# Kernel tuning notes

Measured on AMD Instinct MI355X. Metric: run time of the kernel, lower is better.

## Reference

```python
import jax, jax.numpy as jnp
import numpy as np

N_NODES = 100000
N_EDGES = 1280000
IN_DIM = 64
HID = 64
OUT_DIM = 2
N_GRAPHS = 1000
BN_EPS = 1e-5


def setup_inputs() -> dict:
    key = jax.random.key(0)
    ks = jax.random.split(key, 16)
    x = jax.random.normal(ks[0], (N_NODES, IN_DIM), dtype=jnp.float32)
    edge_index = jax.random.randint(ks[1], (2, N_EDGES), 0, N_NODES, dtype=jnp.int64)
    batch = jnp.sort(jax.random.randint(ks[2], (N_NODES,), 0, N_GRAPHS, dtype=jnp.int64))
    # He-init linear weights (stored as [in, out] so forward is x @ W)
    def he(k, fan_in, fan_out):
        return jax.random.normal(k, (fan_in, fan_out), dtype=jnp.float32) * np.sqrt(2.0 / fan_in)
    return {
        "x": x,
        "edge_index": edge_index,
        "batch": batch,
        "bn_in_g": jnp.ones((IN_DIM,), jnp.float32),
        "bn_in_b": jnp.zeros((IN_DIM,), jnp.float32),
        "W1": he(ks[3], IN_DIM, HID), "b1": jnp.zeros((HID,), jnp.float32),
        "g1": jnp.ones((HID,), jnp.float32), "be1": jnp.zeros((HID,), jnp.float32),
        "W2": he(ks[4], HID, HID), "b2": jnp.zeros((HID,), jnp.float32),
        "g2": jnp.ones((HID,), jnp.float32), "be2": jnp.zeros((HID,), jnp.float32),
        "Wout": he(ks[5], HID, OUT_DIM), "bout": jnp.zeros((OUT_DIM,), jnp.float32),
    }


def _batchnorm(x, g, b):
    # training-mode BN over the node dimension (biased variance, as torch uses for normalization)
    m = jnp.mean(x, axis=0)
    v = jnp.mean(jnp.square(x - m), axis=0)
    return (x - m) * jax.lax.rsqrt(v + BN_EPS) * g + b


def _gcn_norm(edge_index, n):
    # PyG GCNConv normalization with added self-loops:
    # norm_e = deg[src]^-1/2 * deg[dst]^-1/2, deg computed on A + I over targets.
    row = jnp.concatenate([edge_index[0], jnp.arange(n, dtype=edge_index.dtype)])
    col = jnp.concatenate([edge_index[1], jnp.arange(n, dtype=edge_index.dtype)])
    deg = jax.ops.segment_sum(jnp.ones_like(col, dtype=jnp.float32), col, num_segments=n)
    dinv = jnp.where(deg > 0, jax.lax.rsqrt(deg), 0.0)
    norm = dinv[row] * dinv[col]
    return row, col, norm


def _gcn_conv(x, W, b, row, col, norm, n):
    h = x @ W                                   # [N, out]
    msg = h[row] * norm[:, None]                # gather over edges (incl. self-loops)
    agg = jax.ops.segment_sum(msg, col, num_segments=n)
    return agg + b


def reference(x, edge_index, batch, bn_in_g, bn_in_b, W1, b1, g1, be1, W2, b2, g2, be2, Wout, bout):
    n = x.shape[0]
    row, col, norm = _gcn_norm(edge_index, n)
    h = _batchnorm(x, bn_in_g, bn_in_b)         # input BN (dropout = identity in eval)
    h = _gcn_conv(h, W1, b1, row, col, norm, n)
    h = _batchnorm(jax.nn.relu(h), g1, be1)
    h = _gcn_conv(h, W2, b2, row, col, norm, n)
    h = _batchnorm(jax.nn.relu(h), g2, be2)
    # global mean pool per graph
    sums = jax.ops.segment_sum(h, batch, num_segments=N_GRAPHS)
    cnts = jax.ops.segment_sum(jnp.ones((n,), h.dtype), batch, num_segments=N_GRAPHS)
    pooled = sums / jnp.maximum(cnts, 1.0)[:, None]
    return pooled @ Wout + bout                 # [N_GRAPHS, OUT_DIM]
```

## Files before the change

kernel.cpp:

```cpp
#include <hip/hip_runtime.h>
#include <math.h>

#define N_NODES 100000
#define N_EDGES 1280000
#define DIM 64
#define N_GRAPHS 1000
#define BN_EPS 1e-5f
#define NB 392
#define P1B 256
#define P1E 5000
#define SB 400
#define WIN 128
#define NWIN (N_EDGES / WIN)
#define GU 8
#define NSLOT 32

__device__ __forceinline__ unsigned int bf16_rtn2(float a, float b) {
    unsigned int ua = __float_as_uint(a);
    unsigned int ub = __float_as_uint(b);
    ua = (ua + 0x7FFFu + ((ua >> 16) & 1u)) >> 16;
    ub = (ub + 0x7FFFu + ((ub >> 16) & 1u)) >> 16;
    return ua | (ub << 16);
}
__device__ __forceinline__ unsigned short bf16r(float a) {
    unsigned int u = __float_as_uint(a);
    return (unsigned short)((u + 0x7FFFu + ((u >> 16) & 1u)) >> 16);
}
__device__ __forceinline__ float bfup(unsigned short u) {
    return __uint_as_float(((unsigned int)u) << 16);
}

__global__ __launch_bounds__(256) void k_p1hist(const int* __restrict__ ei,
                                                const int* __restrict__ batch,
                                                const float* __restrict__ X,
                                                int* __restrict__ bh,
                                                int* __restrict__ start,
                                                float* __restrict__ gsum,
                                                float* __restrict__ gsumsq) {
    int t = threadIdx.x;
    if (blockIdx.x < P1B) {
        __shared__ int hist[NB];
        for (int b = t; b < NB; b += 256) hist[b] = 0;
        __syncthreads();
        int e0 = blockIdx.x * P1E;
        #pragma unroll 4
        for (int e = e0 + t; e < e0 + P1E; e += 256)
            atomicAdd(&hist[ei[N_EDGES + e] >> 8], 1);
        __syncthreads();
        for (int b = t; b < NB; b += 256) bh[b * P1B + blockIdx.x] = hist[b];
    } else if (blockIdx.x < P1B + SB) {
        int grp = blockIdx.x - P1B;
        int j = t & 63, rg = t >> 6;
        int base = grp * 250;
        float s = 0.f, s2 = 0.f;
        for (int i = base + rg; i < base + 250; i += 4) {
            float v = X[i * DIM + j];
            s += v; s2 += v * v;
        }
        __shared__ float ls[256], ls2[256];
        ls[t] = s; ls2[t] = s2;
        __syncthreads();
        if (t < 64) {
            int slot = (grp & (NSLOT - 1)) * DIM;
            s  = ls[j]  + ls[64 + j]  + ls[128 + j]  + ls[192 + j];
            s2 = ls2[j] + ls2[64 + j] + ls2[128 + j] + ls2[192 + j];
            atomicAdd(&gsum[slot + j], s);
            atomicAdd(&gsumsq[slot + j], s2);
        }
    } else {
        int i = (blockIdx.x - P1B - SB) * 256 + t;
        if (i < N_NODES) {
            int cur = batch[i];
            if (i == 0) { for (int q = 0; q <= cur; q++) start[q] = 0; }
            else {
                int prev = batch[i - 1];
                for (int q = prev + 1; q <= cur; q++) start[q] = i;
            }
            if (i == N_NODES - 1)
                for (int q = cur + 1; q <= N_GRAPHS; q++) start[q] = N_NODES;
        }
    }
}

__global__ void k_scan1(const int* __restrict__ bh, int* __restrict__ iscan,
                        int* __restrict__ bsum) {
    __shared__ int ls[256];
    int i = blockIdx.x * 256 + threadIdx.x;
    int v = bh[i];
    ls[threadIdx.x] = v;
    __syncthreads();
    for (int off = 1; off < 256; off <<= 1) {
        int tv = (threadIdx.x >= off) ? ls[threadIdx.x - off] : 0;
        __syncthreads();
        ls[threadIdx.x] += tv;
        __syncthreads();
    }
    iscan[i] = ls[threadIdx.x];
    if (threadIdx.x == 255) bsum[blockIdx.x] = ls[255];
}

__global__ void k_scan2(const int* __restrict__ bsum, int* __restrict__ boff) {
    __shared__ int ls[512];
    int t = threadIdx.x;
    int v0 = (t < NB) ? bsum[t] : 0;
    ls[t] = v0;
    __syncthreads();
    for (int off = 1; off < 512; off <<= 1) {
        int v = (t >= off) ? ls[t - off] : 0;
        __syncthreads();
        ls[t] += v;
        __syncthreads();
    }
    if (t < NB) boff[t] = ls[t] - v0;
}

__global__ __launch_bounds__(256) void k_p1scat(const int* __restrict__ ei,
                                                const int* __restrict__ bh,
                                                const int* __restrict__ iscan,
                                                const int* __restrict__ boff,
                                                int* __restrict__ tmp) {
    __shared__ int cur[NB];
    int blk = blockIdx.x;
    for (int b = threadIdx.x; b < NB; b += 256) {
        int i = b * P1B + blk;
        cur[b] = boff[b] + iscan[i] - bh[i];
    }
    __syncthreads();
    int e0 = blk * P1E;
    for (int e = e0 + threadIdx.x; e < e0 + P1E; e += 256) {
        int r = ei[e], c = ei[N_EDGES + e];
        int pos = atomicAdd(&cur[c >> 8], 1);
        tmp[pos] = (r << 8) | (c & 255);
    }
}

__global__ __launch_bounds__(256) void k_p2a(const int* __restrict__ tmp,
                                             const int* __restrict__ bh,
                                             const int* __restrict__ iscan,
                                             const int* __restrict__ boff,
                                             int* __restrict__ rowstart,
                                             float* __restrict__ dinv,
                                             int* __restrict__ winnode,
                                             float* __restrict__ C) {
    int b = blockIdx.x, t = threadIdx.x;
    int bstart = boff[b] + iscan[b * 256] - bh[b * 256];
    int bend = (b == NB - 1) ? N_EDGES
                             : (boff[b + 1] + iscan[(b + 1) * 256] - bh[(b + 1) * 256]);
    __shared__ int cnt[256], scn[256];
    cnt[t] = 0;
    __syncthreads();
    for (int e = bstart + t; e < bend; e += 256)
        atomicAdd(&cnt[tmp[e] & 255], 1);
    __syncthreads();
    scn[t] = cnt[t];
    __syncthreads();
    for (int off = 1; off < 256; off <<= 1) {
        int v = (t >= off) ? scn[t - off] : 0;
        __syncthreads();
        scn[t] += v;
        __syncthreads();
    }
    int node = b * 256 + t;
    int deg = cnt[t];
    int rs = bstart + scn[t] - deg;
    bool span = false;
    if (node <= N_NODES) rowstart[node] = rs;
    if (node < N_NODES) {
        dinv[node] = 1.0f / sqrtf((float)(deg + 1));
        int re = rs + deg;
        for (int w = (rs + WIN - 1) / WIN; w * WIN < re; ++w) winnode[w] = node;
        span = (deg > 0) && (rs / WIN != (re - 1) / WIN);
    }
    int lane = t & 63;
    int wbase = b * 256 + (t & ~63);
    unsigned long long m = __ballot(span);
    while (m) {
        int bit = __builtin_ctzll(m);
        m &= m - 1;
        C[(size_t)(wbase + bit) * DIM + lane] = 0.f;
    }
}

__global__ __launch_bounds__(256) void k_p2b(const int* __restrict__ tmp,
                                             const int* __restrict__ bh,
                                             const int* __restrict__ iscan,
                                             const int* __restrict__ boff,
                                             const int* __restrict__ rowstart,
                                             int* __restrict__ csr) {
    int b = blockIdx.x, t = threadIdx.x;
    int bstart = boff[b] + iscan[b * 256] - bh[b * 256];
    int bend = (b == NB - 1) ? N_EDGES
                             : (boff[b + 1] + iscan[(b + 1) * 256] - bh[(b + 1) * 256]);
    __shared__ int curs[256];
    int node = b * 256 + t;
    curs[t] = (node < N_NODES) ? rowstart[node] : 0;
    __syncthreads();
    for (int e = bstart + t; e < bend; e += 256) {
        int rec = tmp[e];
        int pos = atomicAdd(&curs[rec & 255], 1);
        csr[pos] = (int)((unsigned)rec >> 8);
    }
}

__global__ void k_bnfold(float* __restrict__ gsum, float* __restrict__ gsumsq,
                         const float* __restrict__ g, const float* __restrict__ b,
                         const float* __restrict__ W,
                         float* __restrict__ scale, float* __restrict__ cshift) {
    int j = threadIdx.x;
    float ms = 0.f, m2 = 0.f;
    for (int k = 0; k < NSLOT; k++) {
        ms += gsum[k * DIM + j];   gsum[k * DIM + j] = 0.f;
        m2 += gsumsq[k * DIM + j]; gsumsq[k * DIM + j] = 0.f;
    }
    float mean = ms * (1.0f / N_NODES);
    float var  = m2 * (1.0f / N_NODES) - mean * mean;
    float inv  = 1.0f / sqrtf(var + BN_EPS);
    float sc   = g[j] * inv;
    scale[j] = sc;
    __shared__ float shl[64];
    shl[j] = b[j] - mean * sc;
    __syncthreads();
    float s = 0.f;
    for (int k = 0; k < DIM; k++) s += shl[k] * W[k * DIM + j];
    cshift[j] = s;
}

__global__ void k_bnfinal(const float* __restrict__ gsum, const float* __restrict__ gsumsq,
                          const float* __restrict__ g, const float* __restrict__ b,
                          float* __restrict__ scale, float* __restrict__ shift) {
    int j = threadIdx.x;
    float ms = 0.f, m2 = 0.f;
    for (int k = 0; k < NSLOT; k++) { ms += gsum[k * DIM + j]; m2 += gsumsq[k * DIM + j]; }
    float mean = ms * (1.0f / N_NODES);
    float var  = m2 * (1.0f / N_NODES) - mean * mean;
    float inv  = 1.0f / sqrtf(var + BN_EPS);
    float sc   = g[j] * inv;
    scale[j] = sc;
    shift[j] = b[j] - mean * sc;
}

__global__ __launch_bounds__(256) void k_gemm_f32(const float* __restrict__ X,
                                                  const float* __restrict__ W,
                                                  const float* __restrict__ scale,
                                                  const float* __restrict__ cshift,
                                                  const float* __restrict__ dinv,
                                                  unsigned short* __restrict__ T) {
    __shared__ float Wl[64 * 64];
    __shared__ float Al[64 * 65];
    for (int t = threadIdx.x; t < 4096; t += 256) Wl[t] = W[t] * scale[t >> 6];
    int row0 = blockIdx.x * 64;
    for (int t = threadIdx.x; t < 4096; t += 256) {
        int r = t >> 6, k = t & 63;
        int i = row0 + r;
        Al[r * 65 + k] = (i < N_NODES) ? X[(size_t)i * DIM + k] : 0.f;
    }
    __syncthreads();
    int r = threadIdx.x & 63;
    int q = threadIdx.x >> 6;
    float acc[16];
    #pragma unroll
    for (int jj = 0; jj < 16; jj++) acc[jj] = cshift[q * 16 + jj];
    #pragma unroll 4
    for (int k = 0; k < 64; k++) {
        float a = Al[r * 65 + k];
        const float4* wv = (const float4*)&Wl[k * 64 + q * 16];
        float4 w0 = wv[0], w1 = wv[1], w2 = wv[2], w3 = wv[3];
        acc[0]  += a * w0.x; acc[1]  += a * w0.y; acc[2]  += a * w0.z; acc[3]  += a * w0.w;
        acc[4]  += a * w1.x; acc[5]  += a * w1.y; acc[6]  += a * w1.z; acc[7]  += a * w1.w;
        acc[8]  += a * w2.x; acc[9]  += a * w2.y; acc[10] += a * w2.z; acc[11] += a * w2.w;
        acc[12] += a * w3.x; acc[13] += a * w3.y; acc[14] += a * w3.z; acc[15] += a * w3.w;
    }
    int i = row0 + r;
    if (i < N_NODES) {
        float dv = dinv[i];
        unsigned int pk[8];
        #pragma unroll
        for (int jj = 0; jj < 8; jj++)
            pk[jj] = bf16_rtn2(acc[2 * jj] * dv, acc[2 * jj + 1] * dv);
        uint4* outv = (uint4*)&T[(size_t)i * DIM + q * 16];
        outv[0] = make_uint4(pk[0], pk[1], pk[2], pk[3]);
        outv[1] = make_uint4(pk[4], pk[5], pk[6], pk[7]);
    }
}

__global__ __launch_bounds__(256) void k_gemm_b16(const unsigned short* __restrict__ X,
                                                  const float* __restrict__ W,
                                                  const float* __restrict__ scale,
                                                  const float* __restrict__ cshift,
                                                  const float* __restrict__ dinv,
                                                  unsigned short* __restrict__ T) {
    __shared__ float Wl[64 * 64];
    __shared__ float Al[64 * 65];
    for (int t = threadIdx.x; t < 4096; t += 256) Wl[t] = W[t] * scale[t >> 6];
    int row0 = blockIdx.x * 64;
    for (int t = threadIdx.x; t < 4096; t += 256) {
        int r = t >> 6, k = t & 63;
        int i = row0 + r;
        Al[r * 65 + k] = (i < N_NODES) ? bfup(X[(size_t)i * DIM + k]) : 0.f;
    }
    __syncthreads();
    int r = threadIdx.x & 63;
    int q = threadIdx.x >> 6;
    float acc[16];
    #pragma unroll
    for (int jj = 0; jj < 16; jj++) acc[jj] = cshift[q * 16 + jj];
    #pragma unroll 4
    for (int k = 0; k < 64; k++) {
        float a = Al[r * 65 + k];
        const float4* wv = (const float4*)&Wl[k * 64 + q * 16];
        float4 w0 = wv[0], w1 = wv[1], w2 = wv[2], w3 = wv[3];
        acc[0]  += a * w0.x; acc[1]  += a * w0.y; acc[2]  += a * w0.z; acc[3]  += a * w0.w;
        acc[4]  += a * w1.x; acc[5]  += a * w1.y; acc[6]  += a * w1.z; acc[7]  += a * w1.w;
        acc[8]  += a * w2.x; acc[9]  += a * w2.y; acc[10] += a * w2.z; acc[11] += a * w2.w;
        acc[12] += a * w3.x; acc[13] += a * w3.y; acc[14] += a * w3.z; acc[15] += a * w3.w;
    }
    int i = row0 + r;
    if (i < N_NODES) {
        float dv = dinv[i];
        unsigned int pk[8];
        #pragma unroll
        for (int jj = 0; jj < 8; jj++)
            pk[jj] = bf16_rtn2(acc[2 * jj] * dv, acc[2 * jj + 1] * dv);
        uint4* outv = (uint4*)&T[(size_t)i * DIM + q * 16];
        outv[0] = make_uint4(pk[0], pk[1], pk[2], pk[3]);
        outv[1] = make_uint4(pk[4], pk[5], pk[6], pk[7]);
    }
}

__global__ __launch_bounds__(256) void k_gather1(const unsigned short* __restrict__ T,
                                                 const float* __restrict__ dinv,
                                                 const int* __restrict__ rowstart,
                                                 const int* __restrict__ winnode,
                                                 const int* __restrict__ csr,
                                                 const float* __restrict__ bias,
                                                 float* __restrict__ C,
                                                 unsigned short* __restrict__ H,
                                                 float* __restrict__ gsum,
                                                 float* __restrict__ gsumsq) {
    int lane = threadIdx.x & 63;
    int w = blockIdx.x * 4 + (threadIdx.x >> 6);
    float bb = bias[lane];
    float s = 0.f, s2 = 0.f;
    int e = w * WIN;
    const int eend = e + WIN;
    int i  = __builtin_amdgcn_readfirstlane(winnode[w]);
    int re = __builtin_amdgcn_readfirstlane(rowstart[i + 1]);
    bool part = __builtin_amdgcn_readfirstlane(rowstart[i]) < e;
    float acc = 0.f;
    for (; e < eend; e += GU) {
        int src[GU];
        int eu = __builtin_amdgcn_readfirstlane(e);
        #pragma unroll
        for (int u = 0; u < GU; u++) src[u] = csr[eu + u];
        float tv[GU];
        #pragma unroll
        for (int u = 0; u < GU; u++) tv[u] = bfup(T[(size_t)src[u] * DIM + lane]);
        #pragma unroll
        for (int u = 0; u < GU; u++) {
            while (e + u == re) {
                if (part) { atomicAdd(&C[(size_t)i * DIM + lane], acc); part = false; }
                else {
                    float di = dinv[i];
                    float h = fmaxf((acc + bfup(T[(size_t)i * DIM + lane])) * di + bb, 0.f);
                    H[(size_t)i * DIM + lane] = bf16r(h);
                    s += h; s2 += h * h;
                }
                acc = 0.f; ++i;
                re = __builtin_amdgcn_readfirstlane(rowstart[i + 1]);
            }
            acc += tv[u];
        }
    }
    if (part || re > eend) atomicAdd(&C[(size_t)i * DIM + lane], acc);
    else {
        float di = dinv[i];
        float h = fmaxf((acc + bfup(T[(size_t)i * DIM + lane])) * di + bb, 0.f);
        H[(size_t)i * DIM + lane] = bf16r(h);
        s += h; s2 += h * h;
    }
    __shared__ float ls[256], ls2[256];
    ls[threadIdx.x] = s; ls2[threadIdx.x] = s2;
    __syncthreads();
    if (threadIdx.x < 64) {
        int j = threadIdx.x;
        int slot = (blockIdx.x & (NSLOT - 1)) * DIM;
        atomicAdd(&gsum[slot + j],   ls[j] + ls[64 + j] + ls[128 + j] + ls[192 + j]);
        atomicAdd(&gsumsq[slot + j], ls2[j] + ls2[64 + j] + ls2[128 + j] + ls2[192 + j]);
    }
}

__global__ __launch_bounds__(256) void k_gather2(const unsigned short* __restrict__ T,
                                                 const float* __restrict__ dinv,
                                                 const int* __restrict__ rowstart,
                                                 const int* __restrict__ winnode,
                                                 const int* __restrict__ csr,
                                                 const float* __restrict__ bias,
                                                 const int* __restrict__ batch,
                                                 float* __restrict__ C,
                                                 float* __restrict__ pool,
                                                 float* __restrict__ gsum,
                                                 float* __restrict__ gsumsq) {
    int lane = threadIdx.x & 63;
    int w = blockIdx.x * 4 + (threadIdx.x >> 6);
    float bb = bias[lane];
    float s = 0.f, s2 = 0.f, ps = 0.f;
    int cur_g = -1;
    int e = w * WIN;
    const int eend = e + WIN;
    int i  = __builtin_amdgcn_readfirstlane(winnode[w]);
    int re = __builtin_amdgcn_readfirstlane(rowstart[i + 1]);
    bool part = __builtin_amdgcn_readfirstlane(rowstart[i]) < e;
    float acc = 0.f;
    for (; e < eend; e += GU) {
        int src[GU];
        int eu = __builtin_amdgcn_readfirstlane(e);
        #pragma unroll
        for (int u = 0; u < GU; u++) src[u] = csr[eu + u];
        float tv[GU];
        #pragma unroll
        for (int u = 0; u < GU; u++) tv[u] = bfup(T[(size_t)src[u] * DIM + lane]);
        #pragma unroll
        for (int u = 0; u < GU; u++) {
            while (e + u == re) {
                if (part) { atomicAdd(&C[(size_t)i * DIM + lane], acc); part = false; }
                else {
                    float di = dinv[i];
                    float h = fmaxf((acc + bfup(T[(size_t)i * DIM + lane])) * di + bb, 0.f);
                    s += h; s2 += h * h;
                    int g = batch[i];
                    if (g != cur_g) {
                        if (cur_g >= 0) atomicAdd(&pool[(size_t)cur_g * DIM + lane], ps);
                        ps = 0.f; cur_g = g;
                    }
                    ps += h;
                }
                acc = 0.f; ++i;
                re = __builtin_amdgcn_readfirstlane(rowstart[i + 1]);
            }
            acc += tv[u];
        }
    }
    if (part || re > eend) atomicAdd(&C[(size_t)i * DIM + lane], acc);
    else {
        float di = dinv[i];
        float h = fmaxf((acc + bfup(T[(size_t)i * DIM + lane])) * di + bb, 0.f);
        s += h; s2 += h * h;
        int g = batch[i];
        if (g != cur_g) {
            if (cur_g >= 0) atomicAdd(&pool[(size_t)cur_g * DIM + lane], ps);
            ps = 0.f; cur_g = g;
        }
        ps += h;
    }
    if (cur_g >= 0) atomicAdd(&pool[(size_t)cur_g * DIM + lane], ps);
    __shared__ float ls[256], ls2[256];
    ls[threadIdx.x] = s; ls2[threadIdx.x] = s2;
    __syncthreads();
    if (threadIdx.x < 64) {
        int j = threadIdx.x;
        int slot = (blockIdx.x & (NSLOT - 1)) * DIM;
        atomicAdd(&gsum[slot + j],   ls[j] + ls[64 + j] + ls[128 + j] + ls[192 + j]);
        atomicAdd(&gsumsq[slot + j], ls2[j] + ls2[64 + j] + ls2[128 + j] + ls2[192 + j]);
    }
}

__global__ __launch_bounds__(256) void k_strad1(float* __restrict__ C,
                                                const unsigned short* __restrict__ T,
                                                const float* __restrict__ dinv,
                                                const int* __restrict__ rowstart,
                                                const int* __restrict__ winnode,
                                                const float* __restrict__ bias,
                                                unsigned short* __restrict__ H,
                                                float* __restrict__ gsum,
                                                float* __restrict__ gsumsq) {
    int lane = threadIdx.x & 63;
    int wv = threadIdx.x >> 6;
    float bb = bias[lane];
    float s = 0.f, s2 = 0.f;
    __shared__ int anyw;
    if (threadIdx.x == 0) anyw = 0;
    __syncthreads();
    if (blockIdx.x < NWIN / 4) {
        int w = blockIdx.x * 4 + wv;
        int n = winnode[w];
        int rs = rowstart[n];
        if (w == rs / WIN + 1) {
            float di = dinv[n];
            float c = C[(size_t)n * DIM + lane];
            C[(size_t)n * DIM + lane] = 0.f;
            float h = fmaxf((c + bfup(T[(size_t)n * DIM + lane])) * di + bb, 0.f);
            H[(size_t)n * DIM + lane] = bf16r(h);
            s += h; s2 += h * h;
            anyw = 1;
        }
    } else {
        int base = (blockIdx.x - NWIN / 4) * 256 + wv * 64;
        int nb = base + lane;
        int d0 = 0;
        if (nb < N_NODES)
            d0 = (rowstart[nb + 1] == rowstart[nb]) && ((rowstart[nb] & (WIN - 1)) == 0);
        unsigned long long m = __ballot(d0);
        while (m) {
            int b = __builtin_ctzll(m);
            m &= m - 1;
            int n = base + b;
            float di = dinv[n];
            float h = fmaxf(bfup(T[(size_t)n * DIM + lane]) * di + bb, 0.f);
            H[(size_t)n * DIM + lane] = bf16r(h);
            s += h; s2 += h * h;
            anyw = 1;
        }
    }
    __shared__ float ls[256], ls2[256];
    ls[threadIdx.x] = s; ls2[threadIdx.x] = s2;
    __syncthreads();
    if (anyw && threadIdx.x < 64) {
        int j = threadIdx.x;
        int slot = (blockIdx.x & (NSLOT - 1)) * DIM;
        atomicAdd(&gsum[slot + j],   ls[j] + ls[64 + j] + ls[128 + j] + ls[192 + j]);
        atomicAdd(&gsumsq[slot + j], ls2[j] + ls2[64 + j] + ls2[128 + j] + ls2[192 + j]);
    }
}

__global__ __launch_bounds__(256) void k_strad2(const float* __restrict__ C,
                                                const unsigned short* __restrict__ T,
                                                const float* __restrict__ dinv,
                                                const int* __restrict__ rowstart,
                                                const int* __restrict__ winnode,
                                                const float* __restrict__ bias,
                                                const int* __restrict__ batch,
                                                float* __restrict__ pool,
                                                float* __restrict__ gsum,
                                                float* __restrict__ gsumsq) {
    int lane = threadIdx.x & 63;
    int wv = threadIdx.x >> 6;
    float bb = bias[lane];
    float s = 0.f, s2 = 0.f;
    __shared__ int anyw;
    if (threadIdx.x == 0) anyw = 0;
    __syncthreads();
    if (blockIdx.x < NWIN / 4) {
        int w = blockIdx.x * 4 + wv;
        int n = winnode[w];
        int rs = rowstart[n];
        if (w == rs / WIN + 1) {
            float di = dinv[n];
            float h = fmaxf((C[(size_t)n * DIM + lane]
                             + bfup(T[(size_t)n * DIM + lane])) * di + bb, 0.f);
            s += h; s2 += h * h;
            atomicAdd(&pool[(size_t)batch[n] * DIM + lane], h);
            anyw = 1;
        }
    } else {
        int base = (blockIdx.x - NWIN / 4) * 256 + wv * 64;
        int nb = base + lane;
        int d0 = 0;
        if (nb < N_NODES)
            d0 = (rowstart[nb + 1] == rowstart[nb]) && ((rowstart[nb] & (WIN - 1)) == 0);
        unsigned long long m = __ballot(d0);
        while (m) {
            int b = __builtin_ctzll(m);
            m &= m - 1;
            int n = base + b;
            float di = dinv[n];
            float h = fmaxf(bfup(T[(size_t)n * DIM + lane]) * di + bb, 0.f);
            s += h; s2 += h * h;
            atomicAdd(&pool[(size_t)batch[n] * DIM + lane], h);
            anyw = 1;
        }
    }
    __shared__ float ls[256], ls2[256];
    ls[threadIdx.x] = s; ls2[threadIdx.x] = s2;
    __syncthreads();
    if (anyw && threadIdx.x < 64) {
        int j = threadIdx.x;
        int slot = (blockIdx.x & (NSLOT - 1)) * DIM;
        atomicAdd(&gsum[slot + j],   ls[j] + ls[64 + j] + ls[128 + j] + ls[192 + j]);
        atomicAdd(&gsumsq[slot + j], ls2[j] + ls2[64 + j] + ls2[128 + j] + ls2[192 + j]);
    }
}

__global__ void k_final(const float* __restrict__ pool, const int* __restrict__ start,
                        const float* __restrict__ scale, const float* __restrict__ shift,
                        const float* __restrict__ Wout, const float* __restrict__ bout,
                        float* __restrict__ out) {
    int g = blockIdx.x;
    int l = threadIdx.x;
    float c = fmaxf((float)(start[g + 1] - start[g]), 1.f);
    float p = (pool[g * DIM + l] / c) * scale[l] + shift[l];
    float a0 = p * Wout[l * 2 + 0];
    float a1 = p * Wout[l * 2 + 1];
    #pragma unroll
    for (int off = 32; off; off >>= 1) {
        a0 += __shfl_down(a0, off, 64);
        a1 += __shfl_down(a1, off, 64);
    }
    if (l == 0) {
        out[g * 2 + 0] = a0 + bout[0];
        out[g * 2 + 1] = a1 + bout[1];
    }
}

extern "C" void kernel_launch(void* const* d_in, const int* in_sizes, int n_in,
                              void* d_out, int out_size, void* d_ws, size_t ws_size,
                              hipStream_t stream) {
    (void)in_sizes; (void)n_in; (void)out_size; (void)ws_size;
    const float* x       = (const float*)d_in[0];
    const int*   ei      = (const int*)d_in[1];
    const int*   batch   = (const int*)d_in[2];
    const float* bn_in_g = (const float*)d_in[3];
    const float* bn_in_b = (const float*)d_in[4];
    const float* W1      = (const float*)d_in[5];
    const float* b1      = (const float*)d_in[6];
    const float* g1      = (const float*)d_in[7];
    const float* be1     = (const float*)d_in[8];
    const float* W2      = (const float*)d_in[9];
    const float* b2      = (const float*)d_in[10];
    const float* g2      = (const float*)d_in[11];
    const float* be2     = (const float*)d_in[12];
    const float* Wout    = (const float*)d_in[13];
    const float* bout    = (const float*)d_in[14];
    float* out = (float*)d_out;

    char* p = (char*)d_ws;
    float* C = (float*)p;                   p += (size_t)N_NODES * DIM * 4;
    unsigned short* H = (unsigned short*)p; p += (size_t)N_NODES * DIM * 2;
    unsigned short* T = (unsigned short*)p; p += (size_t)N_NODES * DIM * 2;
    int* csr = (int*)p;                     p += (size_t)N_EDGES * 4;
    float* dinv = (float*)p;                p += N_NODES * 4;
    int* bh = (int*)p;                      p += NB * P1B * 4;
    int* iscan = (int*)p;                   p += NB * P1B * 4;
    int* rowstart = (int*)p;                p += (N_NODES + 2) * 4;
    int* winnode = (int*)p;                 p += NWIN * 4;
    int* bsum = (int*)p;                    p += NB * 4;
    int* boff = (int*)p;                    p += NB * 4;
    int* start = (int*)p;                   p += (N_GRAPHS + 2) * 4;
    float* gsum = (float*)p;                p += NSLOT * DIM * 4;
    float* gsumsq = (float*)p;              p += NSLOT * DIM * 4;
    float* scale = (float*)p;               p += DIM * 4;
    float* shift = (float*)p;               p += DIM * 4;
    float* cshift = (float*)p;              p += DIM * 4;
    float* pool = (float*)p;                p += (size_t)N_GRAPHS * DIM * 4;
    int* tmp = (int*)H;

    hipMemsetAsync(gsum, 0, 2 * NSLOT * DIM * sizeof(float), stream);
    hipMemsetAsync(pool, 0, (size_t)N_GRAPHS * DIM * sizeof(float), stream);
    k_p1hist<<<P1B + SB + 392, 256, 0, stream>>>(ei, batch, x, bh, start, gsum, gsumsq);
    k_scan1<<<NB, 256, 0, stream>>>(bh, iscan, bsum);
    k_scan2<<<1, 512, 0, stream>>>(bsum, boff);
    k_p1scat<<<P1B, 256, 0, stream>>>(ei, bh, iscan, boff, tmp);
    k_p2a<<<NB, 256, 0, stream>>>(tmp, bh, iscan, boff, rowstart, dinv, winnode, C);
    k_p2b<<<NB, 256, 0, stream>>>(tmp, bh, iscan, boff, rowstart, csr);

    k_bnfold<<<1, 64, 0, stream>>>(gsum, gsumsq, bn_in_g, bn_in_b, W1, scale, cshift);
    k_gemm_f32<<<(N_NODES + 63) / 64, 256, 0, stream>>>(x, W1, scale, cshift, dinv, T);
    k_gather1<<<NWIN / 4, 256, 0, stream>>>(T, dinv, rowstart, winnode, csr, b1,
                                            C, H, gsum, gsumsq);
    k_strad1<<<NWIN / 4 + 392, 256, 0, stream>>>(C, T, dinv, rowstart, winnode, b1,
                                                 H, gsum, gsumsq);

    k_bnfold<<<1, 64, 0, stream>>>(gsum, gsumsq, g1, be1, W2, scale, cshift);
    k_gemm_b16<<<(N_NODES + 63) / 64, 256, 0, stream>>>(H, W2, scale, cshift, dinv, T);
    k_gather2<<<NWIN / 4, 256, 0, stream>>>(T, dinv, rowstart, winnode, csr, b2,
                                            batch, C, pool, gsum, gsumsq);
    k_strad2<<<NWIN / 4 + 392, 256, 0, stream>>>(C, T, dinv, rowstart, winnode, b2,
                                                 batch, pool, gsum, gsumsq);

    k_bnfinal<<<1, 64, 0, stream>>>(gsum, gsumsq, g2, be2, scale, shift);
    k_final<<<N_GRAPHS, 64, 0, stream>>>(pool, start, scale, shift, Wout, bout, out);
}
```

Baseline: 329.8 us.

## Gather four edges per wave with 8-byte lane loads and preloaded row metadata

The gather kernels now split each wave into four 16-lane groups. Each group handles a different edge and loads 4 bf16 features as one uint2, so one wave covers four edges per load and the partial sums are combined with cross-lane shuffles. CSR indices are loaded once per window and spread with ds_swizzle. rowstart, dinv and batch for the next 64 nodes are preloaded and read with readlane instead of scalar loads. The window shrinks to 64 edges, doubling the number of waves, which adds more straddle atomics and more complex per-edge branching in exchange for fewer, wider memory requests.

```diff
diff --git a/kernel.cpp b/kernel.cpp
--- a/kernel.cpp
+++ b/kernel.cpp
@@ -10,9 +10,8 @@
 #define P1B 256
 #define P1E 5000
 #define SB 400
-#define WIN 128
+#define WIN 64
 #define NWIN (N_EDGES / WIN)
-#define GU 8
 #define NSLOT 32
 
 __device__ __forceinline__ unsigned int bf16_rtn2(float a, float b) {
@@ -29,6 +28,8 @@
 __device__ __forceinline__ float bfup(unsigned short u) {
     return __uint_as_float(((unsigned int)u) << 16);
 }
+__device__ __forceinline__ float blo(unsigned int v) { return __uint_as_float(v << 16); }
+__device__ __forceinline__ float bhi(unsigned int v) { return __uint_as_float(v & 0xFFFF0000u); }
 
 __global__ __launch_bounds__(256) void k_p1hist(const int* __restrict__ ei,
                                                 const int* __restrict__ batch,
@@ -165,6 +166,7 @@
     int rs = bstart + scn[t] - deg;
     bool span = false;
     if (node <= N_NODES) rowstart[node] = rs;
+    if (node == N_NODES) rowstart[node + 1] = rs;
     if (node < N_NODES) {
         dinv[node] = 1.0f / sqrtf((float)(deg + 1));
         int re = rs + deg;
@@ -327,6 +329,48 @@
     }
 }
 
+
+#define SWZ(S) __builtin_amdgcn_ds_swizzle(csrv, (((S) << 5) | 0x10))
+
+#define ISSUE(SRCV, TVV, B) do {                                      \
+    SRCV[0] = SWZ(4 * (B) + 0); SRCV[1] = SWZ(4 * (B) + 1);           \
+    SRCV[2] = SWZ(4 * (B) + 2); SRCV[3] = SWZ(4 * (B) + 3);           \
+    TVV[0] = T2[(unsigned)SRCV[0] * 16u + cc];                        \
+    TVV[1] = T2[(unsigned)SRCV[1] * 16u + cc];                        \
+    TVV[2] = T2[(unsigned)SRCV[2] * 16u + cc];                        \
+    TVV[3] = T2[(unsigned)SRCV[3] * 16u + cc];                        \
+} while (0)
+
+#define STEP(TVV, U, B) do {                                          \
+    const int ebs = e0 + 16 * (B) + 4 * (U);                          \
+    uint2 tvv = TVV[U];                                               \
+    if (re > ebs + 3) {                                               \
+        acc0 += blo(tvv.x); acc1 += bhi(tvv.x);                       \
+        acc2 += blo(tvv.y); acc3 += bhi(tvv.y);                       \
+    } else {                                                          \
+        float a0 = blo(tvv.x), a1 = bhi(tvv.x);                       \
+        float a2 = blo(tvv.y), a3 = bhi(tvv.y);                       \
+        while (re == ebs + 0) FLUSH();                                \
+        if (gg == 0) { acc0 += a0; acc1 += a1; acc2 += a2; acc3 += a3; } \
+        while (re == ebs + 1) FLUSH();                                \
+        if (gg == 1) { acc0 += a0; acc1 += a1; acc2 += a2; acc3 += a3; } \
+        while (re == ebs + 2) FLUSH();                                \
+        if (gg == 2) { acc0 += a0; acc1 += a1; acc2 += a2; acc3 += a3; } \
+        while (re == ebs + 3) FLUSH();                                \
+        if (gg == 3) { acc0 += a0; acc1 += a1; acc2 += a2; acc3 += a3; } \
+    }                                                                 \
+} while (0)
+
+#define CONSUME(TVV, B) do {                                          \
+    STEP(TVV, 0, B); STEP(TVV, 1, B); STEP(TVV, 2, B); STEP(TVV, 3, B); \
+} while (0)
+
+#define COMBINE4()                                                    \
+    float t0 = acc0 + __shfl_xor(acc0, 16); t0 += __shfl_xor(t0, 32); \
+    float t1 = acc1 + __shfl_xor(acc1, 16); t1 += __shfl_xor(t1, 32); \
+    float t2 = acc2 + __shfl_xor(acc2, 16); t2 += __shfl_xor(t2, 32); \
+    float t3 = acc3 + __shfl_xor(acc3, 16); t3 += __shfl_xor(t3, 32);
+
 __global__ __launch_bounds__(256) void k_gather1(const unsigned short* __restrict__ T,
                                                  const float* __restrict__ dinv,
                                                  const int* __restrict__ rowstart,
@@ -337,55 +381,97 @@
                                                  unsigned short* __restrict__ H,
                                                  float* __restrict__ gsum,
                                                  float* __restrict__ gsumsq) {
-    int lane = threadIdx.x & 63;
-    int w = blockIdx.x * 4 + (threadIdx.x >> 6);
-    float bb = bias[lane];
-    float s = 0.f, s2 = 0.f;
-    int e = w * WIN;
-    const int eend = e + WIN;
-    int i  = __builtin_amdgcn_readfirstlane(winnode[w]);
-    int re = __builtin_amdgcn_readfirstlane(rowstart[i + 1]);
-    bool part = __builtin_amdgcn_readfirstlane(rowstart[i]) < e;
-    float acc = 0.f;
-    for (; e < eend; e += GU) {
-        int src[GU];
-        int eu = __builtin_amdgcn_readfirstlane(e);
-        #pragma unroll
-        for (int u = 0; u < GU; u++) src[u] = csr[eu + u];
-        float tv[GU];
-        #pragma unroll
-        for (int u = 0; u < GU; u++) tv[u] = bfup(T[(size_t)src[u] * DIM + lane]);
-        #pragma unroll
-        for (int u = 0; u < GU; u++) {
-            while (e + u == re) {
-                if (part) { atomicAdd(&C[(size_t)i * DIM + lane], acc); part = false; }
-                else {
-                    float di = dinv[i];
-                    float h = fmaxf((acc + bfup(T[(size_t)i * DIM + lane])) * di + bb, 0.f);
-                    H[(size_t)i * DIM + lane] = bf16r(h);
-                    s += h; s2 += h * h;
-                }
-                acc = 0.f; ++i;
-                re = __builtin_amdgcn_readfirstlane(rowstart[i + 1]);
+    const int lane = threadIdx.x & 63;
+    const int gg = lane >> 4;
+    const int cc = lane & 15;
+    const int w = blockIdx.x * 4 + (threadIdx.x >> 6);
+    const int e0 = w * WIN;
+    const int eend = e0 + WIN;
+    const uint2* T2 = (const uint2*)T;
+
+    int csrv = csr[e0 + 4 * cc + gg];
+    int i0 = __builtin_amdgcn_readfirstlane(winnode[w]);
+    int rsv = rowstart[min(i0 + lane, N_NODES + 1)];
+    float dv = dinv[min(i0 + lane, N_NODES - 1)];
+    uint2 tsv = T2[(unsigned)i0 * 16u + cc];
+    const float4 bb = ((const float4*)bias)[cc];
+
+    int i = i0, k = 1;
+    int re = __builtin_amdgcn_readlane(rsv, 1);
+    bool part = __builtin_amdgcn_readlane(rsv, 0) < e0;
+    float acc0 = 0.f, acc1 = 0.f, acc2 = 0.f, acc3 = 0.f;
+    float s0 = 0.f, s1 = 0.f, s2 = 0.f, s3 = 0.f;
+    float q0 = 0.f, q1 = 0.f, q2 = 0.f, q3 = 0.f;
+
+    auto FLUSH = [&]() {
+        COMBINE4();
+        if (part) {
+            if (lane < 16) {
+                float* cp = &C[(size_t)i * DIM + 4 * cc];
+                atomicAdd(cp + 0, t0); atomicAdd(cp + 1, t1);
+                atomicAdd(cp + 2, t2); atomicAdd(cp + 3, t3);
             }
-            acc += tv[u];
-        }
-    }
-    if (part || re > eend) atomicAdd(&C[(size_t)i * DIM + lane], acc);
-    else {
-        float di = dinv[i];
-        float h = fmaxf((acc + bfup(T[(size_t)i * DIM + lane])) * di + bb, 0.f);
-        H[(size_t)i * DIM + lane] = bf16r(h);
-        s += h; s2 += h * h;
-    }
-    __shared__ float ls[256], ls2[256];
-    ls[threadIdx.x] = s; ls2[threadIdx.x] = s2;
+            part = false;
+        } else {
+            int cnt = i - i0;
+            float di = (cnt < 64)
+                ? __int_as_float(__builtin_amdgcn_readlane(__float_as_int(dv), cnt))
+                : dinv[i];
+            float h0 = fmaxf((t0 + blo(tsv.x)) * di + bb.x, 0.f);
+            float h1 = fmaxf((t1 + bhi(tsv.x)) * di + bb.y, 0.f);
+            float h2 = fmaxf((t2 + blo(tsv.y)) * di + bb.z, 0.f);
+            float h3 = fmaxf((t3 + bhi(tsv.y)) * di + bb.w, 0.f);
+            if (lane < 16)
+                ((uint2*)H)[(unsigned)i * 16u + cc] =
+                    make_uint2(bf16_rtn2(h0, h1), bf16_rtn2(h2, h3));
+            s0 += h0; s1 += h1; s2 += h2; s3 += h3;
+            q0 += h0 * h0; q1 += h1 * h1; q2 += h2 * h2; q3 += h3 * h3;
+        }
+        acc0 = acc1 = acc2 = acc3 = 0.f;
+        ++i; ++k;
+        re = (k < 64) ? __builtin_amdgcn_readlane(rsv, k)
+                      : __builtin_amdgcn_readfirstlane(rowstart[i + 1]);
+        tsv = T2[(unsigned)i * 16u + cc];
+    };
+
+    int srcA[4], srcB[4];
+    uint2 tva[4], tvb[4];
+    ISSUE(srcA, tva, 0);
+    ISSUE(srcB, tvb, 1);
+    CONSUME(tva, 0);
+    ISSUE(srcA, tva, 2);
+    CONSUME(tvb, 1);
+    ISSUE(srcB, tvb, 3);
+    CONSUME(tva, 2);
+    CONSUME(tvb, 3);
+
+    if (part || re > eend) {
+        COMBINE4();
+        if (lane < 16) {
+            float* cp = &C[(size_t)i * DIM + 4 * cc];
+            atomicAdd(cp + 0, t0); atomicAdd(cp + 1, t1);
+            atomicAdd(cp + 2, t2); atomicAdd(cp + 3, t3);
+        }
+    } else {
+        FLUSH();
+    }
+
+    __shared__ float shs[4][64], shq[4][64];
+    int wv = threadIdx.x >> 6;
+    if (lane < 16) {
+        shs[wv][4 * cc + 0] = s0; shs[wv][4 * cc + 1] = s1;
+        shs[wv][4 * cc + 2] = s2; shs[wv][4 * cc + 3] = s3;
+        shq[wv][4 * cc + 0] = q0; shq[wv][4 * cc + 1] = q1;
+        shq[wv][4 * cc + 2] = q2; shq[wv][4 * cc + 3] = q3;
+    }
     __syncthreads();
     if (threadIdx.x < 64) {
         int j = threadIdx.x;
+        float vs = shs[0][j] + shs[1][j] + shs[2][j] + shs[3][j];
+        float vq = shq[0][j] + shq[1][j] + shq[2][j] + shq[3][j];
         int slot = (blockIdx.x & (NSLOT - 1)) * DIM;
-        atomicAdd(&gsum[slot + j],   ls[j] + ls[64 + j] + ls[128 + j] + ls[192 + j]);
-        atomicAdd(&gsumsq[slot + j], ls2[j] + ls2[64 + j] + ls2[128 + j] + ls2[192 + j]);
+        atomicAdd(&gsum[slot + j], vs);
+        atomicAdd(&gsumsq[slot + j], vq);
     }
 }
 
@@ -400,67 +486,113 @@
                                                  float* __restrict__ pool,
                                                  float* __restrict__ gsum,
                                                  float* __restrict__ gsumsq) {
-    int lane = threadIdx.x & 63;
-    int w = blockIdx.x * 4 + (threadIdx.x >> 6);
-    float bb = bias[lane];
-    float s = 0.f, s2 = 0.f, ps = 0.f;
+    const int lane = threadIdx.x & 63;
+    const int gg = lane >> 4;
+    const int cc = lane & 15;
+    const int w = blockIdx.x * 4 + (threadIdx.x >> 6);
+    const int e0 = w * WIN;
+    const int eend = e0 + WIN;
+    const uint2* T2 = (const uint2*)T;
+
+    int csrv = csr[e0 + 4 * cc + gg];
+    int i0 = __builtin_amdgcn_readfirstlane(winnode[w]);
+    int rsv = rowstart[min(i0 + lane, N_NODES + 1)];
+    float dv = dinv[min(i0 + lane, N_NODES - 1)];
+    int bv = batch[min(i0 + lane, N_NODES - 1)];
+    uint2 tsv = T2[(unsigned)i0 * 16u + cc];
+    const float4 bb = ((const float4*)bias)[cc];
+
+    int i = i0, k = 1;
+    int re = __builtin_amdgcn_readlane(rsv, 1);
+    bool part = __builtin_amdgcn_readlane(rsv, 0) < e0;
+    float acc0 = 0.f, acc1 = 0.f, acc2 = 0.f, acc3 = 0.f;
+    float s0 = 0.f, s1 = 0.f, s2 = 0.f, s3 = 0.f;
+    float q0 = 0.f, q1 = 0.f, q2 = 0.f, q3 = 0.f;
+    float ps0 = 0.f, ps1 = 0.f, ps2 = 0.f, ps3 = 0.f;
     int cur_g = -1;
-    int e = w * WIN;
-    const int eend = e + WIN;
-    int i  = __builtin_amdgcn_readfirstlane(winnode[w]);
-    int re = __builtin_amdgcn_readfirstlane(rowstart[i + 1]);
-    bool part = __builtin_amdgcn_readfirstlane(rowstart[i]) < e;
-    float acc = 0.f;
-    for (; e < eend; e += GU) {
-        int src[GU];
-        int eu = __builtin_amdgcn_readfirstlane(e);
-        #pragma unroll
-        for (int u = 0; u < GU; u++) src[u] = csr[eu + u];
-        float tv[GU];
-        #pragma unroll
-        for (int u = 0; u < GU; u++) tv[u] = bfup(T[(size_t)src[u] * DIM + lane]);
-        #pragma unroll
-        for (int u = 0; u < GU; u++) {
-            while (e + u == re) {
-                if (part) { atomicAdd(&C[(size_t)i * DIM + lane], acc); part = false; }
-                else {
-                    float di = dinv[i];
-                    float h = fmaxf((acc + bfup(T[(size_t)i * DIM + lane])) * di + bb, 0.f);
-                    s += h; s2 += h * h;
-                    int g = batch[i];
-                    if (g != cur_g) {
-                        if (cur_g >= 0) atomicAdd(&pool[(size_t)cur_g * DIM + lane], ps);
-                        ps = 0.f; cur_g = g;
-                    }
-                    ps += h;
+
+    auto FLUSH = [&]() {
+        COMBINE4();
+        if (part) {
+            if (lane < 16) {
+                float* cp = &C[(size_t)i * DIM + 4 * cc];
+                atomicAdd(cp + 0, t0); atomicAdd(cp + 1, t1);
+                atomicAdd(cp + 2, t2); atomicAdd(cp + 3, t3);
+            }
+            part = false;
+        } else {
+            int cnt = i - i0;
+            float di = (cnt < 64)
+                ? __int_as_float(__builtin_amdgcn_readlane(__float_as_int(dv), cnt))
+                : dinv[i];
+            float h0 = fmaxf((t0 + blo(tsv.x)) * di + bb.x, 0.f);
+            float h1 = fmaxf((t1 + bhi(tsv.x)) * di + bb.y, 0.f);
+            float h2 = fmaxf((t2 + blo(tsv.y)) * di + bb.z, 0.f);
+            float h3 = fmaxf((t3 + bhi(tsv.y)) * di + bb.w, 0.f);
+            s0 += h0; s1 += h1; s2 += h2; s3 += h3;
+            q0 += h0 * h0; q1 += h1 * h1; q2 += h2 * h2; q3 += h3 * h3;
+            int gi = (cnt < 64) ? __builtin_amdgcn_readlane(bv, cnt) : batch[i];
+            if (gi != cur_g) {
+                if (cur_g >= 0 && lane < 16) {
+                    float* pp = &pool[(size_t)cur_g * DIM + 4 * cc];
+                    atomicAdd(pp + 0, ps0); atomicAdd(pp + 1, ps1);
+                    atomicAdd(pp + 2, ps2); atomicAdd(pp + 3, ps3);
                 }
-                acc = 0.f; ++i;
-                re = __builtin_amdgcn_readfirstlane(rowstart[i + 1]);
+                ps0 = ps1 = ps2 = ps3 = 0.f;
+                cur_g = gi;
             }
-            acc += tv[u];
-        }
-    }
-    if (part || re > eend) atomicAdd(&C[(size_t)i * DIM + lane], acc);
-    else {
-        float di = dinv[i];
-        float h = fmaxf((acc + bfup(T[(size_t)i * DIM + lane])) * di + bb, 0.f);
-        s += h; s2 += h * h;
-        int g = batch[i];
-        if (g != cur_g) {
-            if (cur_g >= 0) atomicAdd(&pool[(size_t)cur_g * DIM + lane], ps);
-            ps = 0.f; cur_g = g;
-        }
-        ps += h;
-    }
-    if (cur_g >= 0) atomicAdd(&pool[(size_t)cur_g * DIM + lane], ps);
-    __shared__ float ls[256], ls2[256];
-    ls[threadIdx.x] = s; ls2[threadIdx.x] = s2;
+            ps0 += h0; ps1 += h1; ps2 += h2; ps3 += h3;
+        }
+        acc0 = acc1 = acc2 = acc3 = 0.f;
+        ++i; ++k;
+        re = (k < 64) ? __builtin_amdgcn_readlane(rsv, k)
+                      : __builtin_amdgcn_readfirstlane(rowstart[i + 1]);
+        tsv = T2[(unsigned)i * 16u + cc];
+    };
+
+    int srcA[4], srcB[4];
+    uint2 tva[4], tvb[4];
+    ISSUE(srcA, tva, 0);
+    ISSUE(srcB, tvb, 1);
+    CONSUME(tva, 0);
+    ISSUE(srcA, tva, 2);
+    CONSUME(tvb, 1);
+    ISSUE(srcB, tvb, 3);
+    CONSUME(tva, 2);
+    CONSUME(tvb, 3);
+
+    if (part || re > eend) {
+        COMBINE4();
+        if (lane < 16) {
+            float* cp = &C[(size_t)i * DIM + 4 * cc];
+            atomicAdd(cp + 0, t0); atomicAdd(cp + 1, t1);
+            atomicAdd(cp + 2, t2); atomicAdd(cp + 3, t3);
+        }
+    } else {
+        FLUSH();
+    }
+    if (cur_g >= 0 && lane < 16) {
+        float* pp = &pool[(size_t)cur_g * DIM + 4 * cc];
+        atomicAdd(pp + 0, ps0); atomicAdd(pp + 1, ps1);
+        atomicAdd(pp + 2, ps2); atomicAdd(pp + 3, ps3);
+    }
+
+    __shared__ float shs[4][64], shq[4][64];
+    int wv = threadIdx.x >> 6;
+    if (lane < 16) {
+        shs[wv][4 * cc + 0] = s0; shs[wv][4 * cc + 1] = s1;
+        shs[wv][4 * cc + 2] = s2; shs[wv][4 * cc + 3] = s3;
+        shq[wv][4 * cc + 0] = q0; shq[wv][4 * cc + 1] = q1;
+        shq[wv][4 * cc + 2] = q2; shq[wv][4 * cc + 3] = q3;
+    }
     __syncthreads();
     if (threadIdx.x < 64) {
         int j = threadIdx.x;
+        float vs = shs[0][j] + shs[1][j] + shs[2][j] + shs[3][j];
+        float vq = shq[0][j] + shq[1][j] + shq[2][j] + shq[3][j];
         int slot = (blockIdx.x & (NSLOT - 1)) * DIM;
-        atomicAdd(&gsum[slot + j],   ls[j] + ls[64 + j] + ls[128 + j] + ls[192 + j]);
-        atomicAdd(&gsumsq[slot + j], ls2[j] + ls2[64 + j] + ls2[128 + j] + ls2[192 + j]);
+        atomicAdd(&gsum[slot + j], vs);
+        atomicAdd(&gsumsq[slot + j], vq);
     }
 }
 
```

After: 376.0 us. 14.0% more time.
